# Performance work log

Hardware: AMD Instinct MI355X
Metric: run time of the kernel (lower is better)

The kernel has to match this reference:

```python
import jax, jax.numpy as jnp
import numpy as np

N_NODES = 100000
N_EDGES = 600000
N_FEAT = 128
N_HID = 128
N_GRAPHS = 256


def gcn_conv(x, src, dst, W, b, n_nodes):
    # PyG GCNConv: h = x @ W; add self-loops; sym-normalize; scatter-add; + bias
    h = x @ W  # [N, H]
    loop = jnp.arange(n_nodes)
    s = jnp.concatenate([src, loop])
    d = jnp.concatenate([dst, loop])
    deg = jax.ops.segment_sum(jnp.ones_like(d, dtype=h.dtype), d, num_segments=n_nodes)
    dinv = jnp.where(deg > 0, jax.lax.rsqrt(deg), 0.0)
    norm = dinv[s] * dinv[d]  # [E+N]
    msg = h[s] * norm[:, None]  # gather + scale
    out = jax.ops.segment_sum(msg, d, num_segments=n_nodes)  # scatter-add
    return out + b


def setup_inputs() -> dict:
    key = jax.random.key(0)
    ks = jax.random.split(key, 12)
    x = jax.random.normal(ks[0], (N_NODES, N_FEAT), dtype=jnp.float32)
    edge_index = jax.random.randint(ks[1], (2, N_EDGES), 0, N_NODES, dtype=jnp.int64)
    batch = jnp.sort(jax.random.randint(ks[2], (N_NODES,), 0, N_GRAPHS, dtype=jnp.int64))
    def lin(k, fi, fo):
        s = 1.0 / np.sqrt(fi)
        return jax.random.uniform(k, (fi, fo), jnp.float32, -s, s)
    params = {
        'W1': lin(ks[3], N_FEAT, N_HID), 'b1': jnp.zeros((N_HID,), jnp.float32),
        'W2': lin(ks[4], N_HID, N_HID), 'b2': jnp.zeros((N_HID,), jnp.float32),
        'W3': lin(ks[5], N_HID, N_HID), 'b3': jnp.zeros((N_HID,), jnp.float32),
        'W4': lin(ks[6], N_HID, N_HID), 'b4': jnp.zeros((N_HID,), jnp.float32),
        'Ws1': lin(ks[7], N_HID, N_HID), 'bs1': jnp.zeros((N_HID,), jnp.float32),
        'Ws2': lin(ks[8], N_HID, 1), 'bs2': jnp.zeros((1,), jnp.float32),
    }
    return {'x': x, 'edge_index': edge_index, 'batch': batch, **params}


def reference(x, edge_index, batch, W1, b1, W2, b2, W3, b3, W4, b4, Ws1, bs1, Ws2, bs2):
    src, dst = edge_index[0], edge_index[1]
    h = x
    # 2 conv blocks = 4 GCNConv layers, each followed by ReLU
    for W, b in ((W1, b1), (W2, b2), (W3, b3), (W4, b4)):
        h = jax.nn.relu(gcn_conv(h, src, dst, W, b, N_NODES))
    # global mean pool over nodes per graph
    sums = jax.ops.segment_sum(h, batch, num_segments=N_GRAPHS)  # [G, H]
    cnt = jax.ops.segment_sum(jnp.ones((h.shape[0],), h.dtype), batch, num_segments=N_GRAPHS)
    pooled = sums / jnp.maximum(cnt, 1.0)[:, None]
    # summary MLP: Linear -> ReLU -> Linear(->1)
    out = jax.nn.relu(pooled @ Ws1 + bs1) @ Ws2 + bs2  # [G, 1]
    return out
```

## Files before the change

kernel.cpp:

```cpp
#include <hip/hip_runtime.h>

#define N_NODES 100000
#define N_EDGES 600000
#define NF 128
#define NG 256

typedef _Float16 f16;
typedef f16 half8 __attribute__((ext_vector_type(8)));
typedef f16 half4v __attribute__((ext_vector_type(4)));
typedef float float4v __attribute__((ext_vector_type(4)));


__global__ void k_count(const int* __restrict__ ei, int* __restrict__ counts) {
    int e = blockIdx.x * 256 + threadIdx.x;
    if (e < N_EDGES) atomicAdd(&counts[ei[N_EDGES + e]], 1);
}

__global__ void k_scan1(const int* __restrict__ counts, int* __restrict__ row_ptr,
                        int* __restrict__ bsums, float* __restrict__ dinv) {
    __shared__ int s[256];
    int b = blockIdx.x, t = threadIdx.x;
    int base = b * 2048 + t * 8;
    int local[8];
    int sum = 0;
#pragma unroll
    for (int q = 0; q < 8; q++) {
        int idx = base + q;
        int v = (idx < N_NODES) ? counts[idx] : 0;
        if (idx < N_NODES) dinv[idx] = 1.0f / sqrtf((float)(v + 1));
        local[q] = sum;
        sum += v;
    }
    s[t] = sum;
    __syncthreads();
    for (int off = 1; off < 256; off <<= 1) {
        int v = 0;
        if (t >= off) v = s[t - off];
        __syncthreads();
        s[t] += v;
        __syncthreads();
    }
    int excl = s[t] - sum;
#pragma unroll
    for (int q = 0; q < 8; q++) {
        int idx = base + q;
        if (idx < N_NODES) row_ptr[idx] = excl + local[q];
    }
    if (t == 255) bsums[b] = s[255];
}

__global__ void k_scan3(int* __restrict__ row_ptr, const int* __restrict__ bsums,
                        int* __restrict__ cursor) {
    __shared__ int pre;
    if (threadIdx.x == 0) {
        int g = blockIdx.x >> 3;
        int s = 0;
        for (int j = 0; j < g; j++) s += bsums[j];
        pre = s;
    }
    __syncthreads();
    int i = blockIdx.x * 256 + threadIdx.x;
    if (i < N_NODES) {
        int v = row_ptr[i] + pre;
        row_ptr[i] = v;
        cursor[i] = v;
        if (i == 0) row_ptr[N_NODES] = N_EDGES;
    }
}

__global__ void k_fill(const int* __restrict__ ei, int* __restrict__ cursor,
                       const float* __restrict__ dinv, int2* __restrict__ edge2,
                       const float* __restrict__ W1, const float* __restrict__ W2,
                       const float* __restrict__ W3, const float* __restrict__ W4,
                       f16* __restrict__ wtH, f16* __restrict__ wtL) {
    int e = blockIdx.x * 256 + threadIdx.x;
    if (e < N_EDGES) {
        int src = ei[e];
        int d = ei[N_EDGES + e];
        int p = atomicAdd(&cursor[d], 1);
        edge2[p] = make_int2(src, __float_as_int(dinv[src]));
    }
    if (blockIdx.x < 256) {
        int idx = blockIdx.x * 256 + threadIdx.x;
        int layer = idx >> 14;
        int rem = idx & 16383;
        int n = rem >> 7, k = rem & 127;
        const float* W = (layer == 0) ? W1 : (layer == 1) ? W2 : (layer == 2) ? W3 : W4;
        float w = W[k * NF + n];
        f16 h = (f16)w;
        f16 l = (f16)(w - (float)h);
        wtH[layer * 16384 + n * NF + k] = h;
        wtL[layer * 16384 + n * NF + k] = l;
    }
}


template <int XIN>
__global__ __launch_bounds__(256) void k_gemm_mfma(
    const float* __restrict__ X, const f16* __restrict__ A,
    const f16* __restrict__ WTH, const f16* __restrict__ WTL,
    f16* __restrict__ Z, int M) {
    __shared__ __align__(16) f16 As[64 * 136];

    const int t = threadIdx.x;
    const int row0 = blockIdx.x * 64;
    const int wave = t >> 6;
    const int lane = t & 63;
    const int nl = lane & 15;
    const int quad = lane >> 4;

    half8 fbh[4][2], fbl[4][2];
#pragma unroll
    for (int s = 0; s < 4; s++)
#pragma unroll
        for (int ct = 0; ct < 2; ct++) {
            int ng = wave * 32 + ct * 16 + nl;
            size_t wo = (size_t)ng * NF + s * 32 + quad * 8;
            fbh[s][ct] = *(const half8*)(WTH + wo);
            fbl[s][ct] = *(const half8*)(WTL + wo);
        }

    if (XIN) {
#pragma unroll
        for (int q = 0; q < 8; q++) {
            int lin = t + q * 256;
            int r = lin >> 5, c4 = lin & 31;
            float4 v = make_float4(0.f, 0.f, 0.f, 0.f);
            if (row0 + r < M) v = ((const float4*)(X + (size_t)(row0 + r) * NF))[c4];
            half4v hv = {(f16)v.x, (f16)v.y, (f16)v.z, (f16)v.w};
            *(half4v*)&As[r * 136 + c4 * 4] = hv;
        }
    } else {
#pragma unroll
        for (int q = 0; q < 4; q++) {
            int lin = t + q * 256;
            int r = lin >> 4, c8 = lin & 15;
            half8 v = {};
            if (row0 + r < M) v = *(const half8*)(A + (size_t)(row0 + r) * NF + c8 * 8);
            *(half8*)&As[r * 136 + c8 * 8] = v;
        }
    }
    __syncthreads();

    float4v acc[2][4];
#pragma unroll
    for (int ct = 0; ct < 2; ct++)
#pragma unroll
        for (int rt = 0; rt < 4; rt++) acc[ct][rt] = (float4v)0.f;

#pragma unroll
    for (int s = 0; s < 4; s++) {
        half8 fa[4];
#pragma unroll
        for (int rt = 0; rt < 4; rt++)
            fa[rt] = *(half8*)&As[(rt * 16 + nl) * 136 + s * 32 + quad * 8];
#pragma unroll
        for (int ct = 0; ct < 2; ct++)
#pragma unroll
            for (int rt = 0; rt < 4; rt++) {
                acc[ct][rt] = __builtin_amdgcn_mfma_f32_16x16x32_f16(fa[rt], fbh[s][ct], acc[ct][rt], 0, 0, 0);
                acc[ct][rt] = __builtin_amdgcn_mfma_f32_16x16x32_f16(fa[rt], fbl[s][ct], acc[ct][rt], 0, 0, 0);
            }
    }

    __syncthreads();
#pragma unroll
    for (int ct = 0; ct < 2; ct++)
#pragma unroll
        for (int rt = 0; rt < 4; rt++)
#pragma unroll
            for (int r = 0; r < 4; r++)
                As[(rt * 16 + quad * 4 + r) * 136 + wave * 32 + ct * 16 + nl] =
                    (f16)acc[ct][rt][r];
    __syncthreads();
#pragma unroll
    for (int q = 0; q < 4; q++) {
        int lin = t + q * 256;
        int r = lin >> 4, c8 = lin & 15;
        if (row0 + r < M)
            *(half8*)(Z + (size_t)(row0 + r) * NF + c8 * 8) = *(half8*)&As[r * 136 + c8 * 8];
    }
}


#define ACHUNK 4

__global__ __launch_bounds__(256) void k_agg(const f16* __restrict__ z,
                                             const float* __restrict__ dinv,
                                             const int* __restrict__ row_ptr,
                                             const int2* __restrict__ edge2,
                                             const float* __restrict__ bias,
                                             f16* __restrict__ h) {
    const int t = threadIdx.x;
    const int slot = t >> 4;
    const int fl = t & 15;
    const int sbase = (t & 48);
    const int n0 = (blockIdx.x * 16 + slot) * ACHUNK;
    const half8* z8 = (const half8*)z;

    float bb[8];
    {
        float4 b0 = ((const float4*)bias)[fl * 2];
        float4 b1 = ((const float4*)bias)[fl * 2 + 1];
        bb[0] = b0.x; bb[1] = b0.y; bb[2] = b0.z; bb[3] = b0.w;
        bb[4] = b1.x; bb[5] = b1.y; bb[6] = b1.z; bb[7] = b1.w;
    }

    for (int n = n0; n < n0 + ACHUNK && n < N_NODES; n++) {
        const float di = dinv[n];
        const int beg = row_ptr[n];
        const int end = row_ptr[n + 1];

        float acc[8];
        {
            half8 v = z8[(size_t)n * 16 + fl];
            float w = di * di;
#pragma unroll
            for (int j = 0; j < 8; j++) acc[j] = bb[j] + (float)v[j] * w;
        }

        for (int c = beg; c < end; c += 16) {
            int mcnt = end - c; if (mcnt > 16) mcnt = 16;
            int ce = c + fl;
            int2 ev = (ce < end) ? edge2[ce] : make_int2(n, 0);
            int colv = ev.x;
            float wv = __int_as_float(ev.y);

            int j = 0;
            for (; j + 1 < mcnt; j += 2) {
                int s1 = __shfl(colv, sbase + j, 64);
                float w1 = __shfl(wv, sbase + j, 64) * di;
                int s2 = __shfl(colv, sbase + j + 1, 64);
                float w2 = __shfl(wv, sbase + j + 1, 64) * di;
                half8 v1 = z8[(size_t)s1 * 16 + fl];
                half8 v2 = z8[(size_t)s2 * 16 + fl];
#pragma unroll
                for (int q = 0; q < 8; q++) acc[q] += (float)v1[q] * w1;
#pragma unroll
                for (int q = 0; q < 8; q++) acc[q] += (float)v2[q] * w2;
            }
            if (j < mcnt) {
                int s1 = __shfl(colv, sbase + j, 64);
                float w1 = __shfl(wv, sbase + j, 64) * di;
                half8 v1 = z8[(size_t)s1 * 16 + fl];
#pragma unroll
                for (int q = 0; q < 8; q++) acc[q] += (float)v1[q] * w1;
            }
        }

        half8 o;
#pragma unroll
        for (int j = 0; j < 8; j++) o[j] = (f16)fmaxf(acc[j], 0.f);
        __builtin_nontemporal_store(o, (half8*)h + (size_t)n * 16 + fl);
    }
}


#define POOL_CHUNK 64

__global__ __launch_bounds__(128) void k_pool2(const f16* __restrict__ h,
                                               const int* __restrict__ batch,
                                               float* __restrict__ pooled) {
    int f = threadIdx.x;
    int n0 = blockIdx.x * POOL_CHUNK;
    int n1 = n0 + POOL_CHUNK;
    if (n1 > N_NODES) n1 = N_NODES;
    if (n0 >= N_NODES) return;
    int g = batch[n0];
    float acc = 0.f;
    for (int n = n0; n < n1; n++) {
        int gn = batch[n];
        if (gn != g) {
            atomicAdd(&pooled[g * NF + f], acc);
            acc = 0.f;
            g = gn;
        }
        acc += (float)h[(size_t)n * NF + f];
    }
    atomicAdd(&pooled[g * NF + f], acc);
}


__global__ void k_mlp(const float* __restrict__ pooled, const int* __restrict__ batch,
                      const float* __restrict__ Ws1, const float* __restrict__ bs1,
                      const float* __restrict__ Ws2, const float* __restrict__ bs2,
                      float* __restrict__ out) {
    __shared__ float row[NF];
    __shared__ float red[NF];
    int g = blockIdx.x, f = threadIdx.x;
    int lo = 0, hi = N_NODES;
    while (lo < hi) { int mid = (lo + hi) >> 1; if (batch[mid] < g) lo = mid + 1; else hi = mid; }
    int start = lo;
    hi = N_NODES;
    while (lo < hi) { int mid = (lo + hi) >> 1; if (batch[mid] < g + 1) lo = mid + 1; else hi = mid; }
    float cnt = (float)(lo - start);
    row[f] = pooled[g * NF + f] / fmaxf(cnt, 1.f);
    __syncthreads();
    float t = bs1[f];
    for (int k = 0; k < NF; k++) t += row[k] * Ws1[k * NF + f];
    t = fmaxf(t, 0.f);
    red[f] = t * Ws2[f];
    __syncthreads();
    for (int s = 64; s > 0; s >>= 1) {
        if (f < s) red[f] += red[f + s];
        __syncthreads();
    }
    if (f == 0) out[g] = red[0] + bs2[0];
}


extern "C" void kernel_launch(void* const* d_in, const int* in_sizes, int n_in,
                              void* d_out, int out_size, void* d_ws, size_t ws_size,
                              hipStream_t stream) {
    const float* x    = (const float*)d_in[0];
    const int*   ei   = (const int*)d_in[1];
    const int*   batch= (const int*)d_in[2];
    const float* W1 = (const float*)d_in[3];  const float* b1 = (const float*)d_in[4];
    const float* W2 = (const float*)d_in[5];  const float* b2 = (const float*)d_in[6];
    const float* W3 = (const float*)d_in[7];  const float* b3 = (const float*)d_in[8];
    const float* W4 = (const float*)d_in[9];  const float* b4 = (const float*)d_in[10];
    const float* Ws1= (const float*)d_in[11]; const float* bs1= (const float*)d_in[12];
    const float* Ws2= (const float*)d_in[13]; const float* bs2= (const float*)d_in[14];
    float* out = (float*)d_out;

    char* ws = (char*)d_ws;
    size_t off = 0;
    auto alloc = [&](size_t bytes) {
        void* p = ws + off;
        off += (bytes + 255) & ~(size_t)255;
        return p;
    };
    f16*   bufZ   = (f16*)alloc((size_t)N_NODES * NF * 2);
    f16*   bufH   = (f16*)alloc((size_t)N_NODES * NF * 2);
    f16*   wtH    = (f16*)alloc((size_t)4 * NF * NF * 2);
    f16*   wtL    = (f16*)alloc((size_t)4 * NF * NF * 2);
    int*   counts = (int*)alloc((size_t)N_NODES * 4);
    int*   row_ptr= (int*)alloc((size_t)(N_NODES + 1) * 4);
    int*   cursor = (int*)alloc((size_t)N_NODES * 4);
    int2*  edge2  = (int2*)alloc((size_t)N_EDGES * 8);
    int*   bsums  = (int*)alloc(64 * 4);
    float* dinv   = (float*)alloc((size_t)N_NODES * 4);
    float* pooled = (float*)alloc((size_t)NG * NF * 4);

    hipMemsetAsync(counts, 0, (size_t)N_NODES * 4, stream);
    hipMemsetAsync(pooled, 0, (size_t)NG * NF * 4, stream);
    k_count<<<(N_EDGES + 255) / 256, 256, 0, stream>>>(ei, counts);
    int nscan = (N_NODES + 2047) / 2048;
    k_scan1<<<nscan, 256, 0, stream>>>(counts, row_ptr, bsums, dinv);
    k_scan3<<<(N_NODES + 255) / 256, 256, 0, stream>>>(row_ptr, bsums, cursor);
    k_fill<<<(N_EDGES + 255) / 256, 256, 0, stream>>>(ei, cursor, dinv, edge2,
                                                      W1, W2, W3, W4, wtH, wtL);

    int gblocks = (N_NODES + 63) / 64;
    int ablocks = (N_NODES + 16 * ACHUNK - 1) / (16 * ACHUNK);
    k_gemm_mfma<1><<<gblocks, 256, 0, stream>>>(x, nullptr, wtH, wtL, bufZ, N_NODES);
    k_agg<<<ablocks, 256, 0, stream>>>(bufZ, dinv, row_ptr, edge2, b1, bufH);
    k_gemm_mfma<0><<<gblocks, 256, 0, stream>>>(nullptr, bufH, wtH + 16384, wtL + 16384, bufZ, N_NODES);
    k_agg<<<ablocks, 256, 0, stream>>>(bufZ, dinv, row_ptr, edge2, b2, bufH);
    k_gemm_mfma<0><<<gblocks, 256, 0, stream>>>(nullptr, bufH, wtH + 32768, wtL + 32768, bufZ, N_NODES);
    k_agg<<<ablocks, 256, 0, stream>>>(bufZ, dinv, row_ptr, edge2, b3, bufH);
    k_gemm_mfma<0><<<gblocks, 256, 0, stream>>>(nullptr, bufH, wtH + 49152, wtL + 49152, bufZ, N_NODES);
    k_agg<<<ablocks, 256, 0, stream>>>(bufZ, dinv, row_ptr, edge2, b4, bufH);

    int pblocks = (N_NODES + POOL_CHUNK - 1) / POOL_CHUNK;
    k_pool2<<<pblocks, 128, 0, stream>>>(bufH, batch, pooled);
    k_mlp<<<NG, 128, 0, stream>>>(pooled, batch, Ws1, bs1, Ws2, bs2, out);
}
```

Before: 436.4 us.

## Store CSR column indices only, pre-swizzle weights, drop nontemporal agg stores

The CSR edge array shrinks from (src, dinv[src]) pairs to plain int columns. The aggregation kernel now gathers dinv[col] itself, trading a smaller edge stream and a cheaper fill for an extra random 4-byte gather per edge. Weight halves are written in a per-lane fragment order so each MFMA kernel loads them as contiguous coalesced half8 reads. The aggregation output switches from nontemporal to normal stores, so the next GEMM may find its input in cache.

```diff
diff --git a/kernel.cpp b/kernel.cpp
--- a/kernel.cpp
+++ b/kernel.cpp
@@ -69,28 +69,34 @@
 }
 
 __global__ void k_fill(const int* __restrict__ ei, int* __restrict__ cursor,
-                       const float* __restrict__ dinv, int2* __restrict__ edge2,
+                       int* __restrict__ col,
                        const float* __restrict__ W1, const float* __restrict__ W2,
                        const float* __restrict__ W3, const float* __restrict__ W4,
                        f16* __restrict__ wtH, f16* __restrict__ wtL) {
     int e = blockIdx.x * 256 + threadIdx.x;
     if (e < N_EDGES) {
-        int src = ei[e];
         int d = ei[N_EDGES + e];
         int p = atomicAdd(&cursor[d], 1);
-        edge2[p] = make_int2(src, __float_as_int(dinv[src]));
+        col[p] = ei[e];
     }
     if (blockIdx.x < 256) {
         int idx = blockIdx.x * 256 + threadIdx.x;
         int layer = idx >> 14;
         int rem = idx & 16383;
-        int n = rem >> 7, k = rem & 127;
+        int j = rem & 7;
+        int lane = (rem >> 3) & 63;
+        int chunk = rem >> 9;
+        int wave = chunk >> 3;
+        int s = (chunk >> 1) & 3;
+        int ct = chunk & 1;
+        int n = wave * 32 + ct * 16 + (lane & 15);
+        int k = s * 32 + (lane >> 4) * 8 + j;
         const float* W = (layer == 0) ? W1 : (layer == 1) ? W2 : (layer == 2) ? W3 : W4;
         float w = W[k * NF + n];
         f16 h = (f16)w;
         f16 l = (f16)(w - (float)h);
-        wtH[layer * 16384 + n * NF + k] = h;
-        wtL[layer * 16384 + n * NF + k] = l;
+        wtH[layer * 16384 + rem] = h;
+        wtL[layer * 16384 + rem] = l;
     }
 }
 
@@ -114,8 +120,7 @@
     for (int s = 0; s < 4; s++)
 #pragma unroll
         for (int ct = 0; ct < 2; ct++) {
-            int ng = wave * 32 + ct * 16 + nl;
-            size_t wo = (size_t)ng * NF + s * 32 + quad * 8;
+            size_t wo = (size_t)((((wave * 8 + s * 2 + ct) * 64) + lane) << 3);
             fbh[s][ct] = *(const half8*)(WTH + wo);
             fbl[s][ct] = *(const half8*)(WTL + wo);
         }
@@ -188,7 +193,7 @@
 __global__ __launch_bounds__(256) void k_agg(const f16* __restrict__ z,
                                              const float* __restrict__ dinv,
                                              const int* __restrict__ row_ptr,
-                                             const int2* __restrict__ edge2,
+                                             const int* __restrict__ col,
                                              const float* __restrict__ bias,
                                              f16* __restrict__ h) {
     const int t = threadIdx.x;
@@ -222,16 +227,15 @@
         for (int c = beg; c < end; c += 16) {
             int mcnt = end - c; if (mcnt > 16) mcnt = 16;
             int ce = c + fl;
-            int2 ev = (ce < end) ? edge2[ce] : make_int2(n, 0);
-            int colv = ev.x;
-            float wv = __int_as_float(ev.y);
+            int colv = (ce < end) ? col[ce] : 0;
+            float dvv = dinv[colv];
 
             int j = 0;
             for (; j + 1 < mcnt; j += 2) {
                 int s1 = __shfl(colv, sbase + j, 64);
-                float w1 = __shfl(wv, sbase + j, 64) * di;
+                float w1 = __shfl(dvv, sbase + j, 64) * di;
                 int s2 = __shfl(colv, sbase + j + 1, 64);
-                float w2 = __shfl(wv, sbase + j + 1, 64) * di;
+                float w2 = __shfl(dvv, sbase + j + 1, 64) * di;
                 half8 v1 = z8[(size_t)s1 * 16 + fl];
                 half8 v2 = z8[(size_t)s2 * 16 + fl];
 #pragma unroll
@@ -241,7 +245,7 @@
             }
             if (j < mcnt) {
                 int s1 = __shfl(colv, sbase + j, 64);
-                float w1 = __shfl(wv, sbase + j, 64) * di;
+                float w1 = __shfl(dvv, sbase + j, 64) * di;
                 half8 v1 = z8[(size_t)s1 * 16 + fl];
 #pragma unroll
                 for (int q = 0; q < 8; q++) acc[q] += (float)v1[q] * w1;
@@ -251,7 +255,7 @@
         half8 o;
 #pragma unroll
         for (int j = 0; j < 8; j++) o[j] = (f16)fmaxf(acc[j], 0.f);
-        __builtin_nontemporal_store(o, (half8*)h + (size_t)n * 16 + fl);
+        ((half8*)h)[(size_t)n * 16 + fl] = o;
     }
 }
 
@@ -337,7 +341,7 @@
     int*   counts = (int*)alloc((size_t)N_NODES * 4);
     int*   row_ptr= (int*)alloc((size_t)(N_NODES + 1) * 4);
     int*   cursor = (int*)alloc((size_t)N_NODES * 4);
-    int2*  edge2  = (int2*)alloc((size_t)N_EDGES * 8);
+    int*   col    = (int*)alloc((size_t)N_EDGES * 4);
     int*   bsums  = (int*)alloc(64 * 4);
     float* dinv   = (float*)alloc((size_t)N_NODES * 4);
     float* pooled = (float*)alloc((size_t)NG * NF * 4);
@@ -348,19 +352,19 @@
     int nscan = (N_NODES + 2047) / 2048;
     k_scan1<<<nscan, 256, 0, stream>>>(counts, row_ptr, bsums, dinv);
     k_scan3<<<(N_NODES + 255) / 256, 256, 0, stream>>>(row_ptr, bsums, cursor);
-    k_fill<<<(N_EDGES + 255) / 256, 256, 0, stream>>>(ei, cursor, dinv, edge2,
+    k_fill<<<(N_EDGES + 255) / 256, 256, 0, stream>>>(ei, cursor, col,
                                                       W1, W2, W3, W4, wtH, wtL);
 
     int gblocks = (N_NODES + 63) / 64;
     int ablocks = (N_NODES + 16 * ACHUNK - 1) / (16 * ACHUNK);
     k_gemm_mfma<1><<<gblocks, 256, 0, stream>>>(x, nullptr, wtH, wtL, bufZ, N_NODES);
-    k_agg<<<ablocks, 256, 0, stream>>>(bufZ, dinv, row_ptr, edge2, b1, bufH);
+    k_agg<<<ablocks, 256, 0, stream>>>(bufZ, dinv, row_ptr, col, b1, bufH);
     k_gemm_mfma<0><<<gblocks, 256, 0, stream>>>(nullptr, bufH, wtH + 16384, wtL + 16384, bufZ, N_NODES);
-    k_agg<<<ablocks, 256, 0, stream>>>(bufZ, dinv, row_ptr, edge2, b2, bufH);
+    k_agg<<<ablocks, 256, 0, stream>>>(bufZ, dinv, row_ptr, col, b2, bufH);
     k_gemm_mfma<0><<<gblocks, 256, 0, stream>>>(nullptr, bufH, wtH + 32768, wtL + 32768, bufZ, N_NODES);
-    k_agg<<<ablocks, 256, 0, stream>>>(bufZ, dinv, row_ptr, edge2, b3, bufH);
+    k_agg<<<ablocks, 256, 0, stream>>>(bufZ, dinv, row_ptr, col, b3, bufH);
     k_gemm_mfma<0><<<gblocks, 256, 0, stream>>>(nullptr, bufH, wtH + 49152, wtL + 49152, bufZ, N_NODES);
-    k_agg<<<ablocks, 256, 0, stream>>>(bufZ, dinv, row_ptr, edge2, b4, bufH);
+    k_agg<<<ablocks, 256, 0, stream>>>(bufZ, dinv, row_ptr, col, b4, bufH);
 
     int pblocks = (N_NODES + POOL_CHUNK - 1) / POOL_CHUNK;
     k_pool2<<<pblocks, 128, 0, stream>>>(bufH, batch, pooled);
```

Result: faster. 392.2 us (-10.1%).
